# Kernel tuning notes

Hardware: AMD Instinct MI355X
Metric: run time of the kernel (lower is better)

Reference implementation:

```python
import jax, jax.numpy as jnp
import numpy as np

UNITS = 256
GROUPS = 8
EPS = 1e-3  # keras GroupNormalization default epsilon


def group_norm(x, gamma, beta, groups=GROUPS, eps=EPS):
    # x: [B,H,W,C], normalize per group over (H,W,C//groups)
    B, H, W, C = x.shape
    xg = x.reshape(B, H, W, groups, C // groups)
    mean = xg.mean(axis=(1, 2, 4), keepdims=True)
    var = xg.var(axis=(1, 2, 4), keepdims=True)
    xn = (xg - mean) * jax.lax.rsqrt(var + eps)
    xn = xn.reshape(B, H, W, C)
    return xn * gamma + beta


def setup_inputs() -> dict:
    key = jax.random.key(0)
    ks = jax.random.split(key, 10)
    B, H, W, C = 4, 64, 64, UNITS
    s = 1.0 / np.sqrt(C)
    x = jax.random.normal(ks[0], (B, H, W, C), dtype=jnp.float32)
    return {
        "x": x,
        "gamma": jnp.ones((C,), jnp.float32),
        "beta": jnp.zeros((C,), jnp.float32),
        "Wq": jax.random.uniform(ks[1], (C, C), jnp.float32, -s, s),
        "bq": jnp.zeros((C,), jnp.float32),
        "Wk": jax.random.uniform(ks[2], (C, C), jnp.float32, -s, s),
        "bk": jnp.zeros((C,), jnp.float32),
        "Wv": jax.random.uniform(ks[3], (C, C), jnp.float32, -s, s),
        "bv": jnp.zeros((C,), jnp.float32),
        # proj kernel init scale ~0 -> near-zero weights; use tiny random for nontrivial grads
        "Wp": jax.random.uniform(ks[4], (C, C), jnp.float32, -1e-5, 1e-5),
        "bp": jnp.zeros((C,), jnp.float32),
    }


def reference(x, gamma, beta, Wq, bq, Wk, bk, Wv, bv, Wp, bp):
    B, H, W, C = x.shape
    scale = jnp.float32(C) ** -0.5
    xn = group_norm(x, gamma, beta)  # [B,H,W,C]
    n = H * W
    xf = xn.reshape(B, n, C)
    q = xf @ Wq + bq  # [B,N,C]
    k = xf @ Wk + bk
    v = xf @ Wv + bv
    attn = jnp.einsum('bnc,bmc->bnm', q, k) * scale  # [B,N,N]
    attn = jax.nn.softmax(attn, axis=-1)
    out = jnp.einsum('bnm,bmc->bnc', attn, v)  # [B,N,C]
    out = out @ Wp + bp
    # NOTE: original code reassigns `inputs = self.norm(inputs)` before the
    # residual, so the skip connection uses the NORMALIZED input.
    return xn + out.reshape(B, H, W, C)
```

## Files before the change

### kernel.cpp

```cpp
#include <hip/hip_runtime.h>
#include <hip/hip_bf16.h>

typedef unsigned short u16;
typedef unsigned char u8;
typedef short short8 __attribute__((ext_vector_type(8)));
typedef float floatx4 __attribute__((ext_vector_type(4)));
typedef long long i64;

#define BB 4
#define NN 4096
#define CC 256
#define NG 8
#define M_TOT (BB * NN)
#define GN_EPS 1e-3f
#define ATT_SCALE 0.0625f
#define MCONST 2.5f

__device__ __forceinline__ u16 f2bf(float f) {
  __hip_bfloat16 h = __float2bfloat16(f);
  return __builtin_bit_cast(u16, h);
}
__device__ __forceinline__ float bf2f(u16 u) {
  unsigned int i = ((unsigned int)u) << 16;
  return __builtin_bit_cast(float, i);
}
__device__ __forceinline__ unsigned pack2(float a, float b) {
  return (unsigned)f2bf(a) | ((unsigned)f2bf(b) << 16);
}
__device__ __forceinline__ unsigned pk4f8(float a, float b, float c, float d) {
  unsigned v = __builtin_amdgcn_cvt_pk_fp8_f32(a, b, 0, false);
  v = __builtin_amdgcn_cvt_pk_fp8_f32(c, d, v, true);
  return v;
}
__device__ __forceinline__ u8 f8byte(float a) {
  return (u8)(__builtin_amdgcn_cvt_pk_fp8_f32(a, a, 0, false) & 0xFF);
}

typedef __attribute__((address_space(3))) unsigned int lds_u32;
typedef const __attribute__((address_space(1))) unsigned int glb_u32;
#define ASYNC16(g, l) \
  __builtin_amdgcn_global_load_lds((glb_u32*)(g), (lds_u32*)(l), 16, 0, 0)

__global__ void prep_stats(const float* __restrict__ x,
                           const float* __restrict__ Wq, const float* __restrict__ Wk,
                           const float* __restrict__ Wv, const float* __restrict__ Wp,
                           float* __restrict__ part,
                           u16* __restrict__ wqT, u16* __restrict__ wkT,
                           u16* __restrict__ wvT, u16* __restrict__ wpT) {
  __shared__ u16 Ts[64][68];
  int blk = blockIdx.x;
  int t = threadIdx.x;
  if (blk < 512) {
    int b = blk >> 7, chunk = blk & 127;
    const float* p = x + ((size_t)b * NN + chunk * 32) * CC + t;
    float s = 0.f, ss = 0.f;
    for (int i = 0; i < 32; ++i) { float v = p[(size_t)i * CC]; s += v; ss += v * v; }
    for (int off = 1; off < 32; off <<= 1) { s += __shfl_xor(s, off); ss += __shfl_xor(ss, off); }
    if ((t & 31) == 0) {
      int g = t >> 5;
      part[((size_t)blk * NG + g) * 2 + 0] = s;
      part[((size_t)blk * NG + g) * 2 + 1] = ss;
    }
  } else {
    int pid = blk - 512;
    int y = pid >> 4, tile = pid & 15;
    int o0 = (tile >> 2) * 64, c0 = (tile & 3) * 64;
    const float* W = (y == 0) ? Wq : (y == 1) ? Wk : (y == 2) ? Wv : Wp;
    u16* WT = (y == 0) ? wqT : (y == 1) ? wkT : (y == 2) ? wvT : wpT;
    int cl = t >> 4, o4 = t & 15;
    for (int it = 0; it < 4; ++it) {
      int c = cl + it * 16;
      float4 v = *reinterpret_cast<const float4*>(W + (size_t)(c0 + c) * CC + o0 + o4 * 4);
      Ts[c][o4 * 4 + 0] = f2bf(v.x); Ts[c][o4 * 4 + 1] = f2bf(v.y);
      Ts[c][o4 * 4 + 2] = f2bf(v.z); Ts[c][o4 * 4 + 3] = f2bf(v.w);
    }
    __syncthreads();
    int ol = t >> 3, c8 = t & 7;
    for (int it = 0; it < 2; ++it) {
      int o = ol + it * 32;
      uint4 uv;
      uv.x = (unsigned)Ts[c8 * 8 + 0][o] | ((unsigned)Ts[c8 * 8 + 1][o] << 16);
      uv.y = (unsigned)Ts[c8 * 8 + 2][o] | ((unsigned)Ts[c8 * 8 + 3][o] << 16);
      uv.z = (unsigned)Ts[c8 * 8 + 4][o] | ((unsigned)Ts[c8 * 8 + 5][o] << 16);
      uv.w = (unsigned)Ts[c8 * 8 + 6][o] | ((unsigned)Ts[c8 * 8 + 7][o] << 16);
      *reinterpret_cast<uint4*>(WT + (size_t)(o0 + o) * CC + c0 + c8 * 8) = uv;
    }
  }
}

__global__ __launch_bounds__(256) void gn_apply(
    const float* __restrict__ x, const float* __restrict__ gamma,
    const float* __restrict__ beta, const float* __restrict__ part,
    u16* __restrict__ xnb) {
  __shared__ float gnst[16];
  int blk = blockIdx.x;
  int t = threadIdx.x;
  int b = blk >> 7;
  if (t < 64) {
    int g = t >> 3, j = t & 7;
    float s = 0.f, ss = 0.f;
    for (int ch = j; ch < 128; ch += 8) {
      size_t idx = (((size_t)(b * 128 + ch)) * NG + g) * 2;
      s += part[idx]; ss += part[idx + 1];
    }
    for (int off = 1; off < 8; off <<= 1) { s += __shfl_xor(s, off); ss += __shfl_xor(ss, off); }
    if (j == 0) {
      const float cnt = (float)(NN * (CC / NG));
      float mean = s / cnt;
      float var = ss / cnt - mean * mean;
      gnst[g * 2] = mean;
      gnst[g * 2 + 1] = rsqrtf(var + GN_EPS);
    }
  }
  __syncthreads();
  int row0 = blk * 32;
#pragma unroll
  for (int it = 0; it < 8; ++it) {
    int idx = t + it * 256;
    int rl = idx >> 6, c4 = idx & 63;
    int g = c4 >> 3;
    float mean = gnst[g * 2], rstd = gnst[g * 2 + 1];
    size_t gidx = (size_t)(row0 + rl) * 64 + c4;
    float4 v = reinterpret_cast<const float4*>(x)[gidx];
    float4 gm = reinterpret_cast<const float4*>(gamma)[c4];
    float4 bt = reinterpret_cast<const float4*>(beta)[c4];
    ushort4 o;
    o.x = f2bf((v.x - mean) * rstd * gm.x + bt.x);
    o.y = f2bf((v.y - mean) * rstd * gm.y + bt.y);
    o.z = f2bf((v.z - mean) * rstd * gm.z + bt.z);
    o.w = f2bf((v.w - mean) * rstd * gm.w + bt.w);
    reinterpret_cast<ushort4*>(xnb)[gidx] = o;
  }
}

#define LDT 72
__global__ __launch_bounds__(256) void gemm_qkv(
    const u16* __restrict__ xnb,
    const u16* __restrict__ wqT, const u16* __restrict__ wkT, const u16* __restrict__ wvT,
    const float* __restrict__ bq, const float* __restrict__ bk, const float* __restrict__ bv,
    u8* __restrict__ qb, u8* __restrict__ kb, u8* __restrict__ vTb) {
  __shared__ u16 sm[2 * 128 * LDT];
  u16* Asp = sm;
  u16* Bsp = sm + 128 * LDT;
  int m0 = blockIdx.x * 128;
  int widx = blockIdx.y >> 1;
  int n0 = (blockIdx.y & 1) * 128;
  const u16* wT = (widx == 0) ? wqT : (widx == 1) ? wkT : wvT;
  const float* bias = (widx == 0) ? bq : (widx == 1) ? bk : bv;
  int t = threadIdx.x, w = t >> 6, lane = t & 63, lo = lane & 15, hi = lane >> 4;
  int wm = (w >> 1) * 64, wn = (w & 1) * 64;
  floatx4 acc[4][4];
  for (int i = 0; i < 4; ++i) for (int j = 0; j < 4; ++j) acc[i][j] = (floatx4){0.f, 0.f, 0.f, 0.f};
  for (int kt = 0; kt < 4; ++kt) {
    int k0 = kt * 64;
    __syncthreads();
    for (int i = 0; i < 4; ++i) {
      int idx = t + i * 256, r = idx >> 3, c8 = idx & 7;
      *reinterpret_cast<uint4*>(Asp + r * LDT + c8 * 8) =
          *reinterpret_cast<const uint4*>(xnb + (size_t)(m0 + r) * CC + k0 + c8 * 8);
      *reinterpret_cast<uint4*>(Bsp + r * LDT + c8 * 8) =
          *reinterpret_cast<const uint4*>(wT + (size_t)(n0 + r) * CC + k0 + c8 * 8);
    }
    __syncthreads();
    for (int k32 = 0; k32 < 2; ++k32) {
      short8 af[4], bfr[4];
      for (int mt = 0; mt < 4; ++mt)
        af[mt] = *reinterpret_cast<const short8*>(Asp + (wm + mt * 16 + lo) * LDT + k32 * 32 + hi * 8);
      for (int nt = 0; nt < 4; ++nt)
        bfr[nt] = *reinterpret_cast<const short8*>(Bsp + (wn + nt * 16 + lo) * LDT + k32 * 32 + hi * 8);
      for (int mt = 0; mt < 4; ++mt)
        for (int nt = 0; nt < 4; ++nt)
          acc[mt][nt] = __builtin_amdgcn_mfma_f32_16x16x32_bf16(af[mt], bfr[nt], acc[mt][nt], 0, 0, 0);
    }
  }
  __syncthreads();
  for (int mt = 0; mt < 4; ++mt)
    for (int nt = 0; nt < 4; ++nt)
      for (int r = 0; r < 4; ++r) {
        int rr = wm + mt * 16 + hi * 4 + r;
        int cc2 = wn + nt * 16 + lo;
        sm[rr * 130 + cc2] = f2bf(acc[mt][nt][r] + bias[n0 + cc2]);
      }
  __syncthreads();
  if (widx < 2) {
    u8* outp = (widx == 0) ? qb : kb;
    for (int j = 0; j < 8; ++j) {
      int c = t + j * 256;
      int row = c >> 4, chl = c & 15;
      const u16* sp = sm + row * 130 + chl * 8;
      uint2 val;
      val.x = pk4f8(bf2f(sp[0]), bf2f(sp[1]), bf2f(sp[2]), bf2f(sp[3]));
      val.y = pk4f8(bf2f(sp[4]), bf2f(sp[5]), bf2f(sp[6]), bf2f(sp[7]));
      int rowg = m0 + row;
      int chg = (n0 >> 3) + chl;
      int chs = (widx == 0) ? chg : ((chg + 2 * (rowg & 15)) & 31);
      *reinterpret_cast<uint2*>(outp + (size_t)rowg * CC + chs * 8) = val;
    }
  } else {
    for (int ss = 0; ss < 2; ++ss) {
      int seg = t + ss * 256;
      int dloc = seg & 127, tt = seg >> 7;
      int dglob = n0 + dloc;
      int rot = (dglob >> 1) & 3;
      uint2 arr[4];
      for (int g = 0; g < 4; ++g) {
        int base = tt * 32 + 4 * g;
        unsigned w0 = pk4f8(bf2f(sm[(base + 0) * 130 + dloc]), bf2f(sm[(base + 1) * 130 + dloc]),
                            bf2f(sm[(base + 2) * 130 + dloc]), bf2f(sm[(base + 3) * 130 + dloc]));
        unsigned w1 = pk4f8(bf2f(sm[(base + 16) * 130 + dloc]), bf2f(sm[(base + 17) * 130 + dloc]),
                            bf2f(sm[(base + 18) * 130 + dloc]), bf2f(sm[(base + 19) * 130 + dloc]));
        arr[(g + rot) & 3] = (uint2){w0, w1};
      }
      int tokg = m0 + tt * 32;
      int bb = tokg >> 12, tk = tokg & (NN - 1);
      u8* dst = vTb + ((size_t)(bb * CC + dglob)) * NN + tk;
      *reinterpret_cast<uint4*>(dst) = (uint4){arr[0].x, arr[0].y, arr[1].x, arr[1].y};
      *reinterpret_cast<uint4*>(dst + 16) = (uint4){arr[2].x, arr[2].y, arr[3].x, arr[3].y};
    }
  }
}

__global__ __launch_bounds__(256, 2) void fa_kernel(
    const u8* __restrict__ qb, const u8* __restrict__ kb, const u8* __restrict__ vTb,
    u8* __restrict__ Opart, float* __restrict__ Lpart, u16* __restrict__ aob, int S) {
  __shared__ u8 Ks[32 * 256];
  __shared__ u8 vTs[256 * 32];
  int by = blockIdx.y;
  int b = by / S, split = by - b * S;
  int t = threadIdx.x, w = t >> 6, lane = t & 63, lo = lane & 15, hi = lane >> 4;
  int qw = blockIdx.x * 128 + w * 32;

  i64 qf[2][8];
#pragma unroll
  for (int qg = 0; qg < 2; ++qg) {
    const u8* qrow = qb + ((size_t)(b * NN + qw + qg * 16 + lo)) * CC;
#pragma unroll
    for (int ds = 0; ds < 8; ++ds)
      qf[qg][ds] = *reinterpret_cast<const i64*>(qrow + ds * 32 + hi * 8);
  }
  floatx4 oacc[2][16];
#pragma unroll
  for (int qg = 0; qg < 2; ++qg)
#pragma unroll
    for (int dt = 0; dt < 16; ++dt) oacc[qg][dt] = (floatx4){0.f, 0.f, 0.f, 0.f};
  float lacc[2] = {0.f, 0.f};

  const int TILES = NN / 32;
  int jt0 = split * (TILES / S), jt1 = jt0 + TILES / S;
  const u8* kb_b = kb + (size_t)b * NN * CC;
  const u8* vb_b = vTb + (size_t)b * CC * NN;

  for (int jt = jt0; jt < jt1; ++jt) {
    int j0 = jt * 32;
    __syncthreads();
    {
      const u8* gk = kb_b + (size_t)j0 * CC;
#pragma unroll
      for (int rnd = 0; rnd < 2; ++rnd) {
        int o = (w * 2 + rnd) * 1024;
        ASYNC16(gk + o + lane * 16, Ks + o);
      }
#pragma unroll
      for (int rnd = 0; rnd < 2; ++rnd) {
        int o = (w * 2 + rnd) * 1024;
        int o16 = o + lane * 16;
        const u8* gv = vb_b + (size_t)(o16 >> 5) * NN + j0 + (o16 & 31);
        ASYNC16(gv, vTs + o);
      }
    }
    __syncthreads();

    floatx4 s[2][2];
#pragma unroll
    for (int qg = 0; qg < 2; ++qg)
#pragma unroll
      for (int st = 0; st < 2; ++st) s[qg][st] = (floatx4){0.f, 0.f, 0.f, 0.f};
#pragma unroll
    for (int ds = 0; ds < 8; ++ds) {
      int ch = ds * 4 + hi;
      int pch = (ch + 2 * lo) & 31;
      i64 k0 = *reinterpret_cast<const i64*>(Ks + lo * 256 + pch * 8);
      i64 k1 = *reinterpret_cast<const i64*>(Ks + (16 + lo) * 256 + pch * 8);
#pragma unroll
      for (int qg = 0; qg < 2; ++qg) {
        s[qg][0] = __builtin_amdgcn_mfma_f32_16x16x32_fp8_fp8(k0, qf[qg][ds], s[qg][0], 0, 0, 0);
        s[qg][1] = __builtin_amdgcn_mfma_f32_16x16x32_fp8_fp8(k1, qf[qg][ds], s[qg][1], 0, 0, 0);
      }
    }
    i64 pA[2];
#pragma unroll
    for (int qg = 0; qg < 2; ++qg) {
      float p0 = __expf(fmaf(s[qg][0][0], ATT_SCALE, -MCONST));
      float p1 = __expf(fmaf(s[qg][0][1], ATT_SCALE, -MCONST));
      float p2 = __expf(fmaf(s[qg][0][2], ATT_SCALE, -MCONST));
      float p3 = __expf(fmaf(s[qg][0][3], ATT_SCALE, -MCONST));
      float p4 = __expf(fmaf(s[qg][1][0], ATT_SCALE, -MCONST));
      float p5 = __expf(fmaf(s[qg][1][1], ATT_SCALE, -MCONST));
      float p6 = __expf(fmaf(s[qg][1][2], ATT_SCALE, -MCONST));
      float p7 = __expf(fmaf(s[qg][1][3], ATT_SCALE, -MCONST));
      lacc[qg] += (p0 + p1 + p2 + p3) + (p4 + p5 + p6 + p7);
      uint2 uu;
      uu.x = pk4f8(p0, p1, p2, p3);
      uu.y = pk4f8(p4, p5, p6, p7);
      pA[qg] = __builtin_bit_cast(i64, uu);
    }
#pragma unroll
    for (int dt = 0; dt < 16; ++dt) {
      int d = dt * 16 + lo;
      int gp = (hi + ((d >> 1) & 3)) & 3;
      i64 vf = *reinterpret_cast<const i64*>(vTs + d * 32 + gp * 8);
      oacc[0][dt] = __builtin_amdgcn_mfma_f32_16x16x32_fp8_fp8(pA[0], vf, oacc[0][dt], 0, 0, 0);
      oacc[1][dt] = __builtin_amdgcn_mfma_f32_16x16x32_fp8_fp8(pA[1], vf, oacc[1][dt], 0, 0, 0);
    }
  }

#pragma unroll
  for (int qg = 0; qg < 2; ++qg) {
    lacc[qg] += __shfl_xor(lacc[qg], 16);
    lacc[qg] += __shfl_xor(lacc[qg], 32);
  }

  if (S == 1) {
#pragma unroll
    for (int qg = 0; qg < 2; ++qg) {
      float inv[4];
#pragma unroll
      for (int r = 0; r < 4; ++r) inv[r] = 1.0f / __shfl(lacc[qg], 4 * hi + r);
#pragma unroll
      for (int dt = 0; dt < 16; ++dt)
#pragma unroll
        for (int r = 0; r < 4; ++r) {
          size_t row = (size_t)(b * NN + qw + qg * 16 + 4 * hi + r);
          aob[row * CC + dt * 16 + lo] = f2bf(oacc[qg][dt][r] * inv[r]);
        }
    }
  } else {
    if (hi == 0) {
#pragma unroll
      for (int qg = 0; qg < 2; ++qg)
        Lpart[(size_t)split * M_TOT + b * NN + qw + qg * 16 + lo] = lacc[qg];
    }
    u8* op = Opart + (size_t)split * M_TOT * CC;
#pragma unroll
    for (int qg = 0; qg < 2; ++qg)
#pragma unroll
      for (int dt = 0; dt < 16; ++dt)
#pragma unroll
        for (int r = 0; r < 4; ++r) {
          size_t row = (size_t)(b * NN + qw + qg * 16 + 4 * hi + r);
          op[row * CC + dt * 16 + lo] = f8byte(oacc[qg][dt][r]);
        }
  }
}

__global__ __launch_bounds__(256) void gemm_proj(
    const u16* __restrict__ aob, const u8* __restrict__ Opart,
    const float* __restrict__ Lpart,
    const u16* __restrict__ wpT, const float* __restrict__ bp,
    const u16* __restrict__ xnb, float* __restrict__ out, int S) {
  __shared__ u16 As[64 * LDT];
  __shared__ u16 Bs[128 * LDT];
  __shared__ float linv[64];
  int m0 = blockIdx.x * 64;
  int n0 = blockIdx.y * 128;
  int t = threadIdx.x, w = t >> 6, lane = t & 63, lo = lane & 15, hi = lane >> 4;
  int wm = (w >> 1) * 32, wn = (w & 1) * 64;
  if (S > 1 && t < 64) {
    float l = 0.f;
    for (int sp = 0; sp < S; ++sp) l += Lpart[(size_t)sp * M_TOT + m0 + t];
    linv[t] = 1.f / l;
  }
  floatx4 acc[2][4];
  for (int i = 0; i < 2; ++i) for (int j = 0; j < 4; ++j) acc[i][j] = (floatx4){0.f, 0.f, 0.f, 0.f};
  for (int kt = 0; kt < 4; ++kt) {
    int k0 = kt * 64;
    __syncthreads();
    for (int i = 0; i < 2; ++i) {
      int c = t + i * 256, r = c >> 3, c8 = c & 7;
      if (S == 1) {
        *reinterpret_cast<uint4*>(As + r * LDT + c8 * 8) =
            *reinterpret_cast<const uint4*>(aob + (size_t)(m0 + r) * CC + k0 + c8 * 8);
      } else {
        float f[8] = {0, 0, 0, 0, 0, 0, 0, 0};
        for (int sp = 0; sp < S; ++sp) {
          uint2 uv = *reinterpret_cast<const uint2*>(
              Opart + (size_t)sp * M_TOT * CC + (size_t)(m0 + r) * CC + k0 + c8 * 8);
          f[0] += __builtin_amdgcn_cvt_f32_fp8(uv.x, 0);
          f[1] += __builtin_amdgcn_cvt_f32_fp8(uv.x, 1);
          f[2] += __builtin_amdgcn_cvt_f32_fp8(uv.x, 2);
          f[3] += __builtin_amdgcn_cvt_f32_fp8(uv.x, 3);
          f[4] += __builtin_amdgcn_cvt_f32_fp8(uv.y, 0);
          f[5] += __builtin_amdgcn_cvt_f32_fp8(uv.y, 1);
          f[6] += __builtin_amdgcn_cvt_f32_fp8(uv.y, 2);
          f[7] += __builtin_amdgcn_cvt_f32_fp8(uv.y, 3);
        }
        float iv = linv[r];
        uint4 o;
        o.x = pack2(f[0] * iv, f[1] * iv); o.y = pack2(f[2] * iv, f[3] * iv);
        o.z = pack2(f[4] * iv, f[5] * iv); o.w = pack2(f[6] * iv, f[7] * iv);
        *reinterpret_cast<uint4*>(As + r * LDT + c8 * 8) = o;
      }
    }
    for (int i = 0; i < 4; ++i) {
      int c = t + i * 256, r = c >> 3, c8 = c & 7;
      *reinterpret_cast<uint4*>(Bs + r * LDT + c8 * 8) =
          *reinterpret_cast<const uint4*>(wpT + (size_t)(n0 + r) * CC + k0 + c8 * 8);
    }
    __syncthreads();
    for (int k32 = 0; k32 < 2; ++k32) {
      short8 af[2], bfr[4];
      for (int mt = 0; mt < 2; ++mt)
        af[mt] = *reinterpret_cast<const short8*>(As + (wm + mt * 16 + lo) * LDT + k32 * 32 + hi * 8);
      for (int nt = 0; nt < 4; ++nt)
        bfr[nt] = *reinterpret_cast<const short8*>(Bs + (wn + nt * 16 + lo) * LDT + k32 * 32 + hi * 8);
      for (int mt = 0; mt < 2; ++mt)
        for (int nt = 0; nt < 4; ++nt)
          acc[mt][nt] = __builtin_amdgcn_mfma_f32_16x16x32_bf16(af[mt], bfr[nt], acc[mt][nt], 0, 0, 0);
    }
  }
  for (int mt = 0; mt < 2; ++mt)
    for (int nt = 0; nt < 4; ++nt)
      for (int r = 0; r < 4; ++r) {
        int row = m0 + wm + mt * 16 + hi * 4 + r;
        int col = n0 + wn + nt * 16 + lo;
        size_t o = (size_t)row * CC + col;
        out[o] = acc[mt][nt][r] + bp[col] + bf2f(xnb[o]);
      }
}

extern "C" void kernel_launch(void* const* d_in, const int* in_sizes, int n_in,
                              void* d_out, int out_size, void* d_ws, size_t ws_size,
                              hipStream_t stream) {
  (void)in_sizes; (void)n_in; (void)out_size;
  const float* x     = (const float*)d_in[0];
  const float* gamma = (const float*)d_in[1];
  const float* beta  = (const float*)d_in[2];
  const float* Wq    = (const float*)d_in[3];
  const float* bq    = (const float*)d_in[4];
  const float* Wk    = (const float*)d_in[5];
  const float* bk    = (const float*)d_in[6];
  const float* Wv    = (const float*)d_in[7];
  const float* bv    = (const float*)d_in[8];
  const float* Wp    = (const float*)d_in[9];
  const float* bp    = (const float*)d_in[10];
  float* out = (float*)d_out;

  char* w = (char*)d_ws;
  float* part  = (float*)w;              w += 512 * NG * 2 * 4;
  const size_t SZ = (size_t)M_TOT * CC * 2;
  const size_t SZ8 = (size_t)M_TOT * CC;
  u16* xnb = (u16*)w; w += SZ;
  u8* qb   = (u8*)w;  w += SZ8;
  u8* kb   = (u8*)w;  w += SZ8;
  u8* vTb  = (u8*)w;  w += SZ8;
  u16* aob = (u16*)w; w += SZ;
  u16* wqT = (u16*)w; w += (size_t)CC * CC * 2;
  u16* wkT = (u16*)w; w += (size_t)CC * CC * 2;
  u16* wvT = (u16*)w; w += (size_t)CC * CC * 2;
  u16* wpT = (u16*)w; w += (size_t)CC * CC * 2;

  size_t used = (size_t)(w - (char*)d_ws);
  size_t per_split = SZ8 + (size_t)M_TOT * 4 + 256;
  int S = 4;
  if (used + 4 * per_split > ws_size) S = 2;
  if (used + 2 * per_split > ws_size) S = 1;
  u8* Opart = (u8*)w;                    w += (size_t)S * SZ8;
  float* Lpart = (float*)w;

  prep_stats<<<576, 256, 0, stream>>>(x, Wq, Wk, Wv, Wp, part, wqT, wkT, wvT, wpT);
  gn_apply<<<512, 256, 0, stream>>>(x, gamma, beta, part, xnb);
  gemm_qkv<<<dim3(M_TOT / 128, 6), 256, 0, stream>>>(xnb, wqT, wkT, wvT, bq, bk, bv, qb, kb, vTb);
  fa_kernel<<<dim3(NN / 128, BB * S), 256, 0, stream>>>(qb, kb, vTb, Opart, Lpart, aob, S);
  gemm_proj<<<dim3(M_TOT / 64, 2), 256, 0, stream>>>(aob, Opart, Lpart, wpT, bp, xnb, out, S);
}
```

Measured before the change: 196.8 us.

## Fuse pipeline into one persistent cooperative kernel with grid syncs

Merges the five stage kernels (stats, groupnorm, QKV GEMM, flash attention, projection) into one cooperative persistent kernel. Blocks loop over task ids and a grid-wide sync separates the stages, which removes per-launch overhead and the gaps between kernels. The QKV GEMM tile shrinks to 64 rows so LDS can be shared through a common pool, and the weight transpose now reads global memory directly instead of staging through LDS. The risks are reduced per-stage occupancy (the flash-attention stage is capped at 2 blocks per CU by the launch bounds), the cost of the grid barriers, and a fallback multi-kernel path if the cooperative launch fails.

```diff
diff --git a/kernel.cpp b/kernel.cpp
--- a/kernel.cpp
+++ b/kernel.cpp
@@ -1,5 +1,8 @@
 #include <hip/hip_runtime.h>
 #include <hip/hip_bf16.h>
+#include <hip/hip_cooperative_groups.h>
+
+namespace cg = cooperative_groups;
 
 typedef unsigned short u16;
 typedef unsigned char u8;
@@ -15,6 +18,7 @@
 #define GN_EPS 1e-3f
 #define ATT_SCALE 0.0625f
 #define MCONST 2.5f
+#define LDT 72
 
 __device__ __forceinline__ u16 f2bf(float f) {
   __hip_bfloat16 h = __float2bfloat16(f);
@@ -41,67 +45,62 @@
 #define ASYNC16(g, l) \
   __builtin_amdgcn_global_load_lds((glb_u32*)(g), (lds_u32*)(l), 16, 0, 0)
 
-__global__ void prep_stats(const float* __restrict__ x,
-                           const float* __restrict__ Wq, const float* __restrict__ Wk,
-                           const float* __restrict__ Wv, const float* __restrict__ Wp,
-                           float* __restrict__ part,
-                           u16* __restrict__ wqT, u16* __restrict__ wkT,
-                           u16* __restrict__ wvT, u16* __restrict__ wpT) {
-  __shared__ u16 Ts[64][68];
-  int blk = blockIdx.x;
-  int t = threadIdx.x;
-  if (blk < 512) {
-    int b = blk >> 7, chunk = blk & 127;
-    const float* p = x + ((size_t)b * NN + chunk * 32) * CC + t;
+struct Params {
+  const float* x; const float* gamma; const float* beta;
+  const float* Wq; const float* bq; const float* Wk; const float* bk;
+  const float* Wv; const float* bv; const float* Wp; const float* bp;
+  float* part;
+  u16 *wqT, *wkT, *wvT, *wpT;
+  u16* xnb;
+  u8 *qb, *kb, *vTb;
+  u16* aob;
+  u8* Opart; float* Lpart;
+  float* out;
+  int S;
+};
+
+
+__device__ __forceinline__ void do_stats_task(const Params& P, int task, int t) {
+  if (task < 512) {
+    int b = task >> 7, chunk = task & 127;
+    const float* p = P.x + ((size_t)b * NN + chunk * 32) * CC + t;
     float s = 0.f, ss = 0.f;
     for (int i = 0; i < 32; ++i) { float v = p[(size_t)i * CC]; s += v; ss += v * v; }
     for (int off = 1; off < 32; off <<= 1) { s += __shfl_xor(s, off); ss += __shfl_xor(ss, off); }
     if ((t & 31) == 0) {
       int g = t >> 5;
-      part[((size_t)blk * NG + g) * 2 + 0] = s;
-      part[((size_t)blk * NG + g) * 2 + 1] = ss;
+      P.part[((size_t)task * NG + g) * 2 + 0] = s;
+      P.part[((size_t)task * NG + g) * 2 + 1] = ss;
     }
   } else {
-    int pid = blk - 512;
+    int pid = task - 512;
     int y = pid >> 4, tile = pid & 15;
     int o0 = (tile >> 2) * 64, c0 = (tile & 3) * 64;
-    const float* W = (y == 0) ? Wq : (y == 1) ? Wk : (y == 2) ? Wv : Wp;
-    u16* WT = (y == 0) ? wqT : (y == 1) ? wkT : (y == 2) ? wvT : wpT;
-    int cl = t >> 4, o4 = t & 15;
-    for (int it = 0; it < 4; ++it) {
-      int c = cl + it * 16;
-      float4 v = *reinterpret_cast<const float4*>(W + (size_t)(c0 + c) * CC + o0 + o4 * 4);
-      Ts[c][o4 * 4 + 0] = f2bf(v.x); Ts[c][o4 * 4 + 1] = f2bf(v.y);
-      Ts[c][o4 * 4 + 2] = f2bf(v.z); Ts[c][o4 * 4 + 3] = f2bf(v.w);
-    }
-    __syncthreads();
-    int ol = t >> 3, c8 = t & 7;
-    for (int it = 0; it < 2; ++it) {
-      int o = ol + it * 32;
+    const float* W = (y == 0) ? P.Wq : (y == 1) ? P.Wk : (y == 2) ? P.Wv : P.Wp;
+    u16* WT = (y == 0) ? P.wqT : (y == 1) ? P.wkT : (y == 2) ? P.wvT : P.wpT;
+    int ol = t >> 2, c8 = t & 3;
+    for (int half = 0; half < 2; ++half) {
+      int cbase = c0 + (c8 * 2 + half * 8) * 8;
+      int o = o0 + ol;
       uint4 uv;
-      uv.x = (unsigned)Ts[c8 * 8 + 0][o] | ((unsigned)Ts[c8 * 8 + 1][o] << 16);
-      uv.y = (unsigned)Ts[c8 * 8 + 2][o] | ((unsigned)Ts[c8 * 8 + 3][o] << 16);
-      uv.z = (unsigned)Ts[c8 * 8 + 4][o] | ((unsigned)Ts[c8 * 8 + 5][o] << 16);
-      uv.w = (unsigned)Ts[c8 * 8 + 6][o] | ((unsigned)Ts[c8 * 8 + 7][o] << 16);
-      *reinterpret_cast<uint4*>(WT + (size_t)(o0 + o) * CC + c0 + c8 * 8) = uv;
-    }
-  }
-}
-
-__global__ __launch_bounds__(256) void gn_apply(
-    const float* __restrict__ x, const float* __restrict__ gamma,
-    const float* __restrict__ beta, const float* __restrict__ part,
-    u16* __restrict__ xnb) {
-  __shared__ float gnst[16];
-  int blk = blockIdx.x;
-  int t = threadIdx.x;
-  int b = blk >> 7;
+      unsigned r[8];
+      for (int j = 0; j < 8; ++j)
+        r[j] = (unsigned)f2bf(W[(size_t)(cbase + j) * CC + o]);
+      uv.x = r[0] | (r[1] << 16); uv.y = r[2] | (r[3] << 16);
+      uv.z = r[4] | (r[5] << 16); uv.w = r[6] | (r[7] << 16);
+      *reinterpret_cast<uint4*>(WT + (size_t)o * CC + cbase) = uv;
+    }
+  }
+}
+
+__device__ __forceinline__ void do_gn_task(const Params& P, int task, int t, float* gnst) {
+  int b = task >> 7;
   if (t < 64) {
     int g = t >> 3, j = t & 7;
     float s = 0.f, ss = 0.f;
     for (int ch = j; ch < 128; ch += 8) {
       size_t idx = (((size_t)(b * 128 + ch)) * NG + g) * 2;
-      s += part[idx]; ss += part[idx + 1];
+      s += P.part[idx]; ss += P.part[idx + 1];
     }
     for (int off = 1; off < 8; off <<= 1) { s += __shfl_xor(s, off); ss += __shfl_xor(ss, off); }
     if (j == 0) {
@@ -113,7 +112,7 @@
     }
   }
   __syncthreads();
-  int row0 = blk * 32;
+  int row0 = task * 32;
 #pragma unroll
   for (int it = 0; it < 8; ++it) {
     int idx = t + it * 256;
@@ -121,73 +120,73 @@
     int g = c4 >> 3;
     float mean = gnst[g * 2], rstd = gnst[g * 2 + 1];
     size_t gidx = (size_t)(row0 + rl) * 64 + c4;
-    float4 v = reinterpret_cast<const float4*>(x)[gidx];
-    float4 gm = reinterpret_cast<const float4*>(gamma)[c4];
-    float4 bt = reinterpret_cast<const float4*>(beta)[c4];
+    float4 v = reinterpret_cast<const float4*>(P.x)[gidx];
+    float4 gm = reinterpret_cast<const float4*>(P.gamma)[c4];
+    float4 bt = reinterpret_cast<const float4*>(P.beta)[c4];
     ushort4 o;
     o.x = f2bf((v.x - mean) * rstd * gm.x + bt.x);
     o.y = f2bf((v.y - mean) * rstd * gm.y + bt.y);
     o.z = f2bf((v.z - mean) * rstd * gm.z + bt.z);
     o.w = f2bf((v.w - mean) * rstd * gm.w + bt.w);
-    reinterpret_cast<ushort4*>(xnb)[gidx] = o;
-  }
-}
-
-#define LDT 72
-__global__ __launch_bounds__(256) void gemm_qkv(
-    const u16* __restrict__ xnb,
-    const u16* __restrict__ wqT, const u16* __restrict__ wkT, const u16* __restrict__ wvT,
-    const float* __restrict__ bq, const float* __restrict__ bk, const float* __restrict__ bv,
-    u8* __restrict__ qb, u8* __restrict__ kb, u8* __restrict__ vTb) {
-  __shared__ u16 sm[2 * 128 * LDT];
-  u16* Asp = sm;
-  u16* Bsp = sm + 128 * LDT;
-  int m0 = blockIdx.x * 128;
-  int widx = blockIdx.y >> 1;
-  int n0 = (blockIdx.y & 1) * 128;
-  const u16* wT = (widx == 0) ? wqT : (widx == 1) ? wkT : wvT;
-  const float* bias = (widx == 0) ? bq : (widx == 1) ? bk : bv;
-  int t = threadIdx.x, w = t >> 6, lane = t & 63, lo = lane & 15, hi = lane >> 4;
-  int wm = (w >> 1) * 64, wn = (w & 1) * 64;
-  floatx4 acc[4][4];
-  for (int i = 0; i < 4; ++i) for (int j = 0; j < 4; ++j) acc[i][j] = (floatx4){0.f, 0.f, 0.f, 0.f};
+    reinterpret_cast<ushort4*>(P.xnb)[gidx] = o;
+  }
+  __syncthreads();
+}
+
+__device__ __forceinline__ void do_qkv_task(const Params& P, int task, int t, u16* POOL) {
+  u16* Asp = POOL;
+  u16* Bsp = POOL + 64 * LDT;
+  u16* Cs = POOL;
+  int w = t >> 6, lane = t & 63, lo = lane & 15, hi = lane >> 4;
+  int wm = (w >> 1) * 32, wn = (w & 1) * 64;
+  int m0 = (task & 255) * 64;
+  int rest = task >> 8;
+  int widx = rest >> 1;
+  int n0 = (rest & 1) * 128;
+  const u16* wT = (widx == 0) ? P.wqT : (widx == 1) ? P.wkT : P.wvT;
+  const float* bias = (widx == 0) ? P.bq : (widx == 1) ? P.bk : P.bv;
+  floatx4 acc[2][4];
+  for (int i = 0; i < 2; ++i) for (int j = 0; j < 4; ++j) acc[i][j] = (floatx4){0.f, 0.f, 0.f, 0.f};
   for (int kt = 0; kt < 4; ++kt) {
     int k0 = kt * 64;
     __syncthreads();
+    for (int i = 0; i < 2; ++i) {
+      int c = t + i * 256, r = c >> 3, c8 = c & 7;
+      *reinterpret_cast<uint4*>(Asp + r * LDT + c8 * 8) =
+          *reinterpret_cast<const uint4*>(P.xnb + (size_t)(m0 + r) * CC + k0 + c8 * 8);
+    }
     for (int i = 0; i < 4; ++i) {
-      int idx = t + i * 256, r = idx >> 3, c8 = idx & 7;
-      *reinterpret_cast<uint4*>(Asp + r * LDT + c8 * 8) =
-          *reinterpret_cast<const uint4*>(xnb + (size_t)(m0 + r) * CC + k0 + c8 * 8);
+      int c = t + i * 256, r = c >> 3, c8 = c & 7;
       *reinterpret_cast<uint4*>(Bsp + r * LDT + c8 * 8) =
           *reinterpret_cast<const uint4*>(wT + (size_t)(n0 + r) * CC + k0 + c8 * 8);
     }
     __syncthreads();
     for (int k32 = 0; k32 < 2; ++k32) {
-      short8 af[4], bfr[4];
-      for (int mt = 0; mt < 4; ++mt)
+      short8 af[2], bfr[4];
+      for (int mt = 0; mt < 2; ++mt)
         af[mt] = *reinterpret_cast<const short8*>(Asp + (wm + mt * 16 + lo) * LDT + k32 * 32 + hi * 8);
       for (int nt = 0; nt < 4; ++nt)
         bfr[nt] = *reinterpret_cast<const short8*>(Bsp + (wn + nt * 16 + lo) * LDT + k32 * 32 + hi * 8);
-      for (int mt = 0; mt < 4; ++mt)
+      for (int mt = 0; mt < 2; ++mt)
         for (int nt = 0; nt < 4; ++nt)
           acc[mt][nt] = __builtin_amdgcn_mfma_f32_16x16x32_bf16(af[mt], bfr[nt], acc[mt][nt], 0, 0, 0);
     }
   }
   __syncthreads();
-  for (int mt = 0; mt < 4; ++mt)
+  for (int mt = 0; mt < 2; ++mt)
     for (int nt = 0; nt < 4; ++nt)
       for (int r = 0; r < 4; ++r) {
         int rr = wm + mt * 16 + hi * 4 + r;
         int cc2 = wn + nt * 16 + lo;
-        sm[rr * 130 + cc2] = f2bf(acc[mt][nt][r] + bias[n0 + cc2]);
+        Cs[rr * 130 + cc2] = f2bf(acc[mt][nt][r] + bias[n0 + cc2]);
       }
   __syncthreads();
   if (widx < 2) {
-    u8* outp = (widx == 0) ? qb : kb;
-    for (int j = 0; j < 8; ++j) {
+    u8* outp = (widx == 0) ? P.qb : P.kb;
+    for (int j = 0; j < 4; ++j) {
       int c = t + j * 256;
       int row = c >> 4, chl = c & 15;
-      const u16* sp = sm + row * 130 + chl * 8;
+      const u16* sp = Cs + row * 130 + chl * 8;
       uint2 val;
       val.x = pk4f8(bf2f(sp[0]), bf2f(sp[1]), bf2f(sp[2]), bf2f(sp[3]));
       val.y = pk4f8(bf2f(sp[4]), bf2f(sp[5]), bf2f(sp[6]), bf2f(sp[7]));
@@ -197,43 +196,40 @@
       *reinterpret_cast<uint2*>(outp + (size_t)rowg * CC + chs * 8) = val;
     }
   } else {
-    for (int ss = 0; ss < 2; ++ss) {
-      int seg = t + ss * 256;
-      int dloc = seg & 127, tt = seg >> 7;
-      int dglob = n0 + dloc;
-      int rot = (dglob >> 1) & 3;
-      uint2 arr[4];
-      for (int g = 0; g < 4; ++g) {
-        int base = tt * 32 + 4 * g;
-        unsigned w0 = pk4f8(bf2f(sm[(base + 0) * 130 + dloc]), bf2f(sm[(base + 1) * 130 + dloc]),
-                            bf2f(sm[(base + 2) * 130 + dloc]), bf2f(sm[(base + 3) * 130 + dloc]));
-        unsigned w1 = pk4f8(bf2f(sm[(base + 16) * 130 + dloc]), bf2f(sm[(base + 17) * 130 + dloc]),
-                            bf2f(sm[(base + 18) * 130 + dloc]), bf2f(sm[(base + 19) * 130 + dloc]));
-        arr[(g + rot) & 3] = (uint2){w0, w1};
-      }
-      int tokg = m0 + tt * 32;
-      int bb = tokg >> 12, tk = tokg & (NN - 1);
-      u8* dst = vTb + ((size_t)(bb * CC + dglob)) * NN + tk;
-      *reinterpret_cast<uint4*>(dst) = (uint4){arr[0].x, arr[0].y, arr[1].x, arr[1].y};
-      *reinterpret_cast<uint4*>(dst + 16) = (uint4){arr[2].x, arr[2].y, arr[3].x, arr[3].y};
-    }
-  }
-}
-
-__global__ __launch_bounds__(256, 2) void fa_kernel(
-    const u8* __restrict__ qb, const u8* __restrict__ kb, const u8* __restrict__ vTb,
-    u8* __restrict__ Opart, float* __restrict__ Lpart, u16* __restrict__ aob, int S) {
-  __shared__ u8 Ks[32 * 256];
-  __shared__ u8 vTs[256 * 32];
-  int by = blockIdx.y;
+    int dloc = t & 127, tt = t >> 7;
+    int dglob = n0 + dloc;
+    int rot = (dglob >> 1) & 3;
+    uint2 arr[4];
+    for (int g = 0; g < 4; ++g) {
+      int base = tt * 32 + 4 * g;
+      unsigned w0 = pk4f8(bf2f(Cs[(base + 0) * 130 + dloc]), bf2f(Cs[(base + 1) * 130 + dloc]),
+                          bf2f(Cs[(base + 2) * 130 + dloc]), bf2f(Cs[(base + 3) * 130 + dloc]));
+      unsigned w1 = pk4f8(bf2f(Cs[(base + 16) * 130 + dloc]), bf2f(Cs[(base + 17) * 130 + dloc]),
+                          bf2f(Cs[(base + 18) * 130 + dloc]), bf2f(Cs[(base + 19) * 130 + dloc]));
+      arr[(g + rot) & 3] = (uint2){w0, w1};
+    }
+    int tokg = m0 + tt * 32;
+    int bb = tokg >> 12, tk2 = tokg & (NN - 1);
+    u8* dst = P.vTb + ((size_t)(bb * CC + dglob)) * NN + tk2;
+    *reinterpret_cast<uint4*>(dst) = (uint4){arr[0].x, arr[0].y, arr[1].x, arr[1].y};
+    *reinterpret_cast<uint4*>(dst + 16) = (uint4){arr[2].x, arr[2].y, arr[3].x, arr[3].y};
+  }
+  __syncthreads();
+}
+
+__device__ __forceinline__ void do_fa_task(const Params& P, int task, int t, u8* POOL) {
+  u8* Ks = POOL;
+  u8* vTs = POOL + 8192;
+  int w = t >> 6, lane = t & 63, lo = lane & 15, hi = lane >> 4;
+  int qtile = task & 31, by = task >> 5;
+  int S = P.S;
   int b = by / S, split = by - b * S;
-  int t = threadIdx.x, w = t >> 6, lane = t & 63, lo = lane & 15, hi = lane >> 4;
-  int qw = blockIdx.x * 128 + w * 32;
+  int qw = qtile * 128 + w * 32;
 
   i64 qf[2][8];
 #pragma unroll
   for (int qg = 0; qg < 2; ++qg) {
-    const u8* qrow = qb + ((size_t)(b * NN + qw + qg * 16 + lo)) * CC;
+    const u8* qrow = P.qb + ((size_t)(b * NN + qw + qg * 16 + lo)) * CC;
 #pragma unroll
     for (int ds = 0; ds < 8; ++ds)
       qf[qg][ds] = *reinterpret_cast<const i64*>(qrow + ds * 32 + hi * 8);
@@ -247,8 +243,8 @@
 
   const int TILES = NN / 32;
   int jt0 = split * (TILES / S), jt1 = jt0 + TILES / S;
-  const u8* kb_b = kb + (size_t)b * NN * CC;
-  const u8* vb_b = vTb + (size_t)b * CC * NN;
+  const u8* kb_b = P.kb + (size_t)b * NN * CC;
+  const u8* vb_b = P.vTb + (size_t)b * CC * NN;
 
   for (int jt = jt0; jt < jt1; ++jt) {
     int j0 = jt * 32;
@@ -320,7 +316,7 @@
     lacc[qg] += __shfl_xor(lacc[qg], 32);
   }
 
-  if (S == 1) {
+  if (P.S == 1) {
 #pragma unroll
     for (int qg = 0; qg < 2; ++qg) {
       float inv[4];
@@ -331,16 +327,16 @@
 #pragma unroll
         for (int r = 0; r < 4; ++r) {
           size_t row = (size_t)(b * NN + qw + qg * 16 + 4 * hi + r);
-          aob[row * CC + dt * 16 + lo] = f2bf(oacc[qg][dt][r] * inv[r]);
+          P.aob[row * CC + dt * 16 + lo] = f2bf(oacc[qg][dt][r] * inv[r]);
         }
     }
   } else {
     if (hi == 0) {
 #pragma unroll
       for (int qg = 0; qg < 2; ++qg)
-        Lpart[(size_t)split * M_TOT + b * NN + qw + qg * 16 + lo] = lacc[qg];
-    }
-    u8* op = Opart + (size_t)split * M_TOT * CC;
+        P.Lpart[(size_t)split * M_TOT + b * NN + qw + qg * 16 + lo] = lacc[qg];
+    }
+    u8* op = P.Opart + (size_t)split * M_TOT * CC;
 #pragma unroll
     for (int qg = 0; qg < 2; ++qg)
 #pragma unroll
@@ -351,23 +347,21 @@
           op[row * CC + dt * 16 + lo] = f8byte(oacc[qg][dt][r]);
         }
   }
-}
-
-__global__ __launch_bounds__(256) void gemm_proj(
-    const u16* __restrict__ aob, const u8* __restrict__ Opart,
-    const float* __restrict__ Lpart,
-    const u16* __restrict__ wpT, const float* __restrict__ bp,
-    const u16* __restrict__ xnb, float* __restrict__ out, int S) {
-  __shared__ u16 As[64 * LDT];
-  __shared__ u16 Bs[128 * LDT];
-  __shared__ float linv[64];
-  int m0 = blockIdx.x * 64;
-  int n0 = blockIdx.y * 128;
-  int t = threadIdx.x, w = t >> 6, lane = t & 63, lo = lane & 15, hi = lane >> 4;
+  __syncthreads();
+}
+
+__device__ __forceinline__ void do_proj_task(const Params& P, int task, int t,
+                                             u16* POOL, float* linv) {
+  u16* Asp = POOL;
+  u16* Bsp = POOL + 64 * LDT;
+  int w = t >> 6, lane = t & 63, lo = lane & 15, hi = lane >> 4;
+  int S = P.S;
+  int m0 = (task & 255) * 64;
+  int n0 = (task >> 8) * 128;
   int wm = (w >> 1) * 32, wn = (w & 1) * 64;
   if (S > 1 && t < 64) {
     float l = 0.f;
-    for (int sp = 0; sp < S; ++sp) l += Lpart[(size_t)sp * M_TOT + m0 + t];
+    for (int sp = 0; sp < S; ++sp) l += P.Lpart[(size_t)sp * M_TOT + m0 + t];
     linv[t] = 1.f / l;
   }
   floatx4 acc[2][4];
@@ -378,13 +372,13 @@
     for (int i = 0; i < 2; ++i) {
       int c = t + i * 256, r = c >> 3, c8 = c & 7;
       if (S == 1) {
-        *reinterpret_cast<uint4*>(As + r * LDT + c8 * 8) =
-            *reinterpret_cast<const uint4*>(aob + (size_t)(m0 + r) * CC + k0 + c8 * 8);
+        *reinterpret_cast<uint4*>(Asp + r * LDT + c8 * 8) =
+            *reinterpret_cast<const uint4*>(P.aob + (size_t)(m0 + r) * CC + k0 + c8 * 8);
       } else {
         float f[8] = {0, 0, 0, 0, 0, 0, 0, 0};
         for (int sp = 0; sp < S; ++sp) {
           uint2 uv = *reinterpret_cast<const uint2*>(
-              Opart + (size_t)sp * M_TOT * CC + (size_t)(m0 + r) * CC + k0 + c8 * 8);
+              P.Opart + (size_t)sp * M_TOT * CC + (size_t)(m0 + r) * CC + k0 + c8 * 8);
           f[0] += __builtin_amdgcn_cvt_f32_fp8(uv.x, 0);
           f[1] += __builtin_amdgcn_cvt_f32_fp8(uv.x, 1);
           f[2] += __builtin_amdgcn_cvt_f32_fp8(uv.x, 2);
@@ -398,21 +392,21 @@
         uint4 o;
         o.x = pack2(f[0] * iv, f[1] * iv); o.y = pack2(f[2] * iv, f[3] * iv);
         o.z = pack2(f[4] * iv, f[5] * iv); o.w = pack2(f[6] * iv, f[7] * iv);
-        *reinterpret_cast<uint4*>(As + r * LDT + c8 * 8) = o;
+        *reinterpret_cast<uint4*>(Asp + r * LDT + c8 * 8) = o;
       }
     }
     for (int i = 0; i < 4; ++i) {
       int c = t + i * 256, r = c >> 3, c8 = c & 7;
-      *reinterpret_cast<uint4*>(Bs + r * LDT + c8 * 8) =
-          *reinterpret_cast<const uint4*>(wpT + (size_t)(n0 + r) * CC + k0 + c8 * 8);
+      *reinterpret_cast<uint4*>(Bsp + r * LDT + c8 * 8) =
+          *reinterpret_cast<const uint4*>(P.wpT + (size_t)(n0 + r) * CC + k0 + c8 * 8);
     }
     __syncthreads();
     for (int k32 = 0; k32 < 2; ++k32) {
       short8 af[2], bfr[4];
       for (int mt = 0; mt < 2; ++mt)
-        af[mt] = *reinterpret_cast<const short8*>(As + (wm + mt * 16 + lo) * LDT + k32 * 32 + hi * 8);
+        af[mt] = *reinterpret_cast<const short8*>(Asp + (wm + mt * 16 + lo) * LDT + k32 * 32 + hi * 8);
       for (int nt = 0; nt < 4; ++nt)
-        bfr[nt] = *reinterpret_cast<const short8*>(Bs + (wn + nt * 16 + lo) * LDT + k32 * 32 + hi * 8);
+        bfr[nt] = *reinterpret_cast<const short8*>(Bsp + (wn + nt * 16 + lo) * LDT + k32 * 32 + hi * 8);
       for (int mt = 0; mt < 2; ++mt)
         for (int nt = 0; nt < 4; ++nt)
           acc[mt][nt] = __builtin_amdgcn_mfma_f32_16x16x32_bf16(af[mt], bfr[nt], acc[mt][nt], 0, 0, 0);
@@ -424,52 +418,109 @@
         int row = m0 + wm + mt * 16 + hi * 4 + r;
         int col = n0 + wn + nt * 16 + lo;
         size_t o = (size_t)row * CC + col;
-        out[o] = acc[mt][nt][r] + bp[col] + bf2f(xnb[o]);
+        P.out[o] = acc[mt][nt][r] + P.bp[col] + bf2f(P.xnb[o]);
       }
+  __syncthreads();
+}
+
+__global__ __launch_bounds__(256, 2) void mono(Params P) {
+  cg::grid_group grid = cg::this_grid();
+  __shared__ __align__(16) u16 POOL[(64 + 128) * LDT];
+  __shared__ float gnst[16];
+  __shared__ float linv[64];
+  int t = threadIdx.x;
+  int nb = gridDim.x;
+
+  for (int task = blockIdx.x; task < 576; task += nb) do_stats_task(P, task, t);
+  grid.sync();
+  for (int task = blockIdx.x; task < 512; task += nb) do_gn_task(P, task, t, gnst);
+  grid.sync();
+  for (int task = blockIdx.x; task < 1536; task += nb) do_qkv_task(P, task, t, POOL);
+  grid.sync();
+  for (int task = blockIdx.x; task < 32 * BB * P.S; task += nb) do_fa_task(P, task, t, (u8*)POOL);
+  grid.sync();
+  for (int task = blockIdx.x; task < 512; task += nb) do_proj_task(P, task, t, POOL, linv);
+}
+
+__global__ void fb_stats(Params P) { do_stats_task(P, blockIdx.x, threadIdx.x); }
+__global__ __launch_bounds__(256) void fb_gn(Params P) {
+  __shared__ float gnst[16];
+  do_gn_task(P, blockIdx.x, threadIdx.x, gnst);
+}
+__global__ __launch_bounds__(256) void fb_qkv(Params P) {
+  __shared__ __align__(16) u16 POOL[(64 + 128) * LDT];
+  do_qkv_task(P, blockIdx.x, threadIdx.x, POOL);
+}
+__global__ __launch_bounds__(256, 2) void fb_fa(Params P) {
+  __shared__ __align__(16) u8 POOL[16384];
+  do_fa_task(P, blockIdx.x, threadIdx.x, POOL);
+}
+__global__ __launch_bounds__(256) void fb_proj(Params P) {
+  __shared__ __align__(16) u16 POOL[(64 + 128) * LDT];
+  __shared__ float linv[64];
+  do_proj_task(P, blockIdx.x, threadIdx.x, POOL, linv);
 }
 
 extern "C" void kernel_launch(void* const* d_in, const int* in_sizes, int n_in,
                               void* d_out, int out_size, void* d_ws, size_t ws_size,
                               hipStream_t stream) {
   (void)in_sizes; (void)n_in; (void)out_size;
-  const float* x     = (const float*)d_in[0];
-  const float* gamma = (const float*)d_in[1];
-  const float* beta  = (const float*)d_in[2];
-  const float* Wq    = (const float*)d_in[3];
-  const float* bq    = (const float*)d_in[4];
-  const float* Wk    = (const float*)d_in[5];
-  const float* bk    = (const float*)d_in[6];
-  const float* Wv    = (const float*)d_in[7];
-  const float* bv    = (const float*)d_in[8];
-  const float* Wp    = (const float*)d_in[9];
-  const float* bp    = (const float*)d_in[10];
-  float* out = (float*)d_out;
+  Params P;
+  P.x     = (const float*)d_in[0];
+  P.gamma = (const float*)d_in[1];
+  P.beta  = (const float*)d_in[2];
+  P.Wq    = (const float*)d_in[3];
+  P.bq    = (const float*)d_in[4];
+  P.Wk    = (const float*)d_in[5];
+  P.bk    = (const float*)d_in[6];
+  P.Wv    = (const float*)d_in[7];
+  P.bv    = (const float*)d_in[8];
+  P.Wp    = (const float*)d_in[9];
+  P.bp    = (const float*)d_in[10];
+  P.out = (float*)d_out;
 
   char* w = (char*)d_ws;
-  float* part  = (float*)w;              w += 512 * NG * 2 * 4;
+  P.part = (float*)w;                    w += 512 * NG * 2 * 4;
   const size_t SZ = (size_t)M_TOT * CC * 2;
   const size_t SZ8 = (size_t)M_TOT * CC;
-  u16* xnb = (u16*)w; w += SZ;
-  u8* qb   = (u8*)w;  w += SZ8;
-  u8* kb   = (u8*)w;  w += SZ8;
-  u8* vTb  = (u8*)w;  w += SZ8;
-  u16* aob = (u16*)w; w += SZ;
-  u16* wqT = (u16*)w; w += (size_t)CC * CC * 2;
-  u16* wkT = (u16*)w; w += (size_t)CC * CC * 2;
-  u16* wvT = (u16*)w; w += (size_t)CC * CC * 2;
-  u16* wpT = (u16*)w; w += (size_t)CC * CC * 2;
+  P.xnb = (u16*)w; w += SZ;
+  P.qb  = (u8*)w;  w += SZ8;
+  P.kb  = (u8*)w;  w += SZ8;
+  P.vTb = (u8*)w;  w += SZ8;
+  P.aob = (u16*)w; w += SZ;
+  P.wqT = (u16*)w; w += (size_t)CC * CC * 2;
+  P.wkT = (u16*)w; w += (size_t)CC * CC * 2;
+  P.wvT = (u16*)w; w += (size_t)CC * CC * 2;
+  P.wpT = (u16*)w; w += (size_t)CC * CC * 2;
 
   size_t used = (size_t)(w - (char*)d_ws);
   size_t per_split = SZ8 + (size_t)M_TOT * 4 + 256;
   int S = 4;
   if (used + 4 * per_split > ws_size) S = 2;
   if (used + 2 * per_split > ws_size) S = 1;
-  u8* Opart = (u8*)w;                    w += (size_t)S * SZ8;
-  float* Lpart = (float*)w;
-
-  prep_stats<<<576, 256, 0, stream>>>(x, Wq, Wk, Wv, Wp, part, wqT, wkT, wvT, wpT);
-  gn_apply<<<512, 256, 0, stream>>>(x, gamma, beta, part, xnb);
-  gemm_qkv<<<dim3(M_TOT / 128, 6), 256, 0, stream>>>(xnb, wqT, wkT, wvT, bq, bk, bv, qb, kb, vTb);
-  fa_kernel<<<dim3(NN / 128, BB * S), 256, 0, stream>>>(qb, kb, vTb, Opart, Lpart, aob, S);
-  gemm_proj<<<dim3(M_TOT / 64, 2), 256, 0, stream>>>(aob, Opart, Lpart, wpT, bp, xnb, out, S);
-}
+  P.S = S;
+  P.Opart = (u8*)w;                      w += (size_t)S * SZ8;
+  P.Lpart = (float*)w;
+
+  bool coop_ok = false;
+  int occ = 0;
+  hipError_t oe = hipOccupancyMaxActiveBlocksPerMultiprocessor(&occ, (const void*)mono, 256, 0);
+  if (oe == hipSuccess && occ >= 1) {
+    int nblk = occ * 256;
+    if (nblk > 512) nblk = 512;
+    void* args[] = { &P };
+    hipError_t le = hipLaunchCooperativeKernel((void*)mono, dim3(nblk), dim3(256), args, 0, stream);
+    if (le == hipSuccess) coop_ok = true;
+    else (void)hipGetLastError();
+  } else {
+    (void)hipGetLastError();
+  }
+
+  if (!coop_ok) {
+    fb_stats<<<576, 256, 0, stream>>>(P);
+    fb_gn<<<512, 256, 0, stream>>>(P);
+    fb_qkv<<<1536, 256, 0, stream>>>(P);
+    fb_fa<<<32 * BB * S, 256, 0, stream>>>(P);
+    fb_proj<<<512, 256, 0, stream>>>(P);
+  }
+}
```

New measurement: 404.6 us. +105.6%, slower.
